# Kernel tuning notes

Measured on AMD Instinct MI355X. Metric: run time of the kernel, lower is better.

The kernel has to match this reference:

```python
import jax, jax.numpy as jnp
import numpy as np

UNITS = 50257
CUTOFF = [2000, 10000, UNITS]  # _cutoff = cutoff + [units]
C = 1024                        # channels (d_model)
N = 4096                        # flattened tokens (batch*seq)
N_TAILS = len(CUTOFF) - 1       # 2
ROOT_OUT = CUTOFF[0] + N_TAILS  # 2002
TAIL_DIMS = [256, 64]           # round(C/4**(i+1)/8)*8


def setup_inputs() -> dict:
    key = jax.random.key(0)
    ks = jax.random.split(key, 7)
    logits = jax.random.normal(ks[0], (N, C), jnp.float32)
    targets = jax.random.randint(ks[1], (N,), 0, UNITS, jnp.int32)
    s = 0.02
    head_kernel = jax.random.normal(ks[2], (C, ROOT_OUT), jnp.float32) * s
    proj0 = jax.random.normal(ks[3], (C, TAIL_DIMS[0]), jnp.float32) * s
    scale0 = jax.random.normal(ks[4], (TAIL_DIMS[0], CUTOFF[1] - CUTOFF[0]), jnp.float32) * s
    proj1 = jax.random.normal(ks[5], (C, TAIL_DIMS[1]), jnp.float32) * s
    scale1 = jax.random.normal(ks[6], (TAIL_DIMS[1], CUTOFF[2] - CUTOFF[1]), jnp.float32) * s
    return {"logits": logits, "targets": targets, "head_kernel": head_kernel,
            "proj0": proj0, "scale0": scale0, "proj1": proj1, "scale1": scale1}


def _sparse_ce(lg, labels):
    # sparse softmax cross entropy, numerically stable (single logsumexp)
    lse = jax.nn.logsumexp(lg, axis=-1)
    picked = jnp.take_along_axis(lg, labels[:, None].astype(jnp.int32), axis=1)[:, 0]
    return lse - picked


def reference(logits, targets, head_kernel, proj0, scale0, proj1, scale1):
    # Faithful jax version of AdaptiveSoftmax._train_loss (return_probs=False,
    # dropout=0, no bias on Denses, loss_reduction=SUM_OVER_BATCH_SIZE i.e. mean).
    # Dynamic boolean gather is replaced by dense compute + masked mean, which
    # yields identical math under jit (mean over the routed subset).
    root_logits = (logits @ head_kernel).astype(jnp.float32)  # [N, ROOT_OUT]
    root_targets = targets
    tails = [(proj0, scale0), (proj1, scale1)]
    losses = []
    for i, (p, s) in enumerate(tails):
        lo, hi = CUTOFF[i], CUTOFF[i + 1]
        m = (targets >= lo) & (targets < hi)
        root_targets = jnp.where(m, CUTOFF[0] + i, root_targets)
        tail_logits = ((logits @ p) @ s).astype(jnp.float32)  # [N, hi-lo]
        tail_tgt = jnp.clip(targets - lo, 0, hi - lo - 1)
        ce = _sparse_ce(tail_logits, tail_tgt)
        mf = m.astype(jnp.float32)
        losses.append(jnp.sum(ce * mf) / jnp.maximum(jnp.sum(mf), 1.0))
    root_loss = jnp.mean(_sparse_ce(root_logits, root_targets))
    all_losses = jnp.stack([root_loss] + losses)
    return jnp.mean(all_losses)
```

## Files before the change

kernel.cpp:

```cpp
#include <hip/hip_runtime.h>
#include <math.h>
#include <stdint.h>

#define NROWS 4096
#define CDIM 1024
#define T0_LO 2000
#define T0_HI 10000
#define T1_LO 10000
#define ROOT_COLS 2002
#define ROOT_PAD 2048
#define T0_COLS 8000
#define T0_PAD 8064
#define T1_COLS 40257
#define T1_PAD 40320
#define HB_STRIDE 320
#define LOG2E 1.44269504088896340736f
#define LN2 0.69314718055994530942f

using short8  = __attribute__((ext_vector_type(8))) short;
using ushort8 = __attribute__((ext_vector_type(8))) unsigned short;
using floatx4 = __attribute__((ext_vector_type(4))) float;

__device__ __forceinline__ unsigned short f2bf(float x) {
  union { float f; unsigned int u; } v; v.f = x;
  unsigned int r = v.u + 0x7fffu + ((v.u >> 16) & 1u);
  return (unsigned short)(r >> 16);
}
__device__ __forceinline__ float bf2f(unsigned short h) {
  union { unsigned int u; float f; } v; v.u = ((unsigned int)h) << 16;
  return v.f;
}
__device__ __forceinline__ floatx4 mfma16(short8 a, short8 b, floatx4 c) {
  return __builtin_amdgcn_mfma_f32_16x16x32_bf16(a, b, c, 0, 0, 0);
}
__device__ __forceinline__ void stage16(const unsigned short* g,
                                        unsigned short* lds_wave_base, int lane) {
#if __has_builtin(__builtin_amdgcn_global_load_lds)
  __builtin_amdgcn_global_load_lds(
      (const __attribute__((address_space(1))) void*)g,
      (__attribute__((address_space(3))) void*)lds_wave_base, 16, 0, 0);
#else
  ((ushort8*)lds_wave_base)[lane] = *(const ushort8*)g;
#endif
}

static constexpr size_t B_HB  = 0;
static constexpr size_t B_LB  = B_HB + 4096ull * 320 * 2;
static constexpr size_t B_WP  = B_LB + 4096ull * 1024 * 2;
static constexpr size_t B_WH  = B_WP + 384ull * 1024 * 2;
static constexpr size_t B_WS0 = B_WH + 2048ull * 1024 * 2;
static constexpr size_t B_WS1 = B_WS0 + 8064ull * 256 * 2;
static constexpr size_t B_S   = B_WS1 + 40320ull * 64 * 2;
static constexpr size_t B_P   = B_S + 3ull * 4096 * 4;
static constexpr size_t B_I0  = B_P + 3ull * 4096 * 4;
static constexpr size_t B_I1  = B_I0 + 4096ull * 4;
static constexpr size_t B_CNT = B_I1 + 4096ull * 4;

#define PR_WH_END   2048
#define PR_WP0_END  (PR_WH_END + 256)
#define PR_WP1_END  (PR_WP0_END + 64)
#define PR_WS0_END  (PR_WP1_END + 2016)
#define PR_WS1_END  (PR_WS0_END + 2520)
#define PR_ZERO_END (PR_WS1_END + 32)
#define PR_LB_END   (PR_ZERO_END + 2048)
#define PR_S_END    (PR_LB_END + 4)
#define PR_TOTAL    (PR_S_END + 1)

__global__ __launch_bounds__(256) void prep_kernel(
    const float* __restrict__ head, const float* __restrict__ proj0,
    const float* __restrict__ proj1, const float* __restrict__ scale0,
    const float* __restrict__ scale1, const float* __restrict__ logits,
    const int* __restrict__ targets,
    unsigned short* __restrict__ Wh, unsigned short* __restrict__ Wp,
    unsigned short* __restrict__ Ws0, unsigned short* __restrict__ Ws1,
    unsigned short* __restrict__ Lb, float* __restrict__ S,
    int* __restrict__ idx0, int* __restrict__ idx1, int* __restrict__ cnt) {
  const int id = blockIdx.x, tid = threadIdx.x;
  if (id >= PR_S_END) {
    __shared__ int base[2];
    if (tid < 2) base[tid] = 0;
    __syncthreads();
    for (int n = tid; n < NROWS; n += 256) {
      int t = targets[n];
      if (t >= T0_LO && t < T0_HI) idx0[atomicAdd(&base[0], 1)] = n;
      else if (t >= T1_LO)         idx1[atomicAdd(&base[1], 1)] = n;
    }
    __syncthreads();
    if (tid < 2) cnt[tid] = base[tid];
    return;
  }
  if (id >= PR_LB_END) {
    int rel = id - PR_LB_END;
    float4 z = make_float4(0.f, 0.f, 0.f, 0.f);
#pragma unroll
    for (int j = 0; j < 3; j++)
      ((float4*)S)[rel * 768 + j * 256 + tid] = z;
    return;
  }
  if (id >= PR_ZERO_END) {
    size_t base = (size_t)(id - PR_ZERO_END) * 2048 + tid * 8;
    float4 v0 = *(const float4*)(logits + base);
    float4 v1 = *(const float4*)(logits + base + 4);
    ushort8 h;
    h[0] = f2bf(v0.x); h[1] = f2bf(v0.y); h[2] = f2bf(v0.z); h[3] = f2bf(v0.w);
    h[4] = f2bf(v1.x); h[5] = f2bf(v1.y); h[6] = f2bf(v1.z); h[7] = f2bf(v1.w);
    *(ushort8*)(Lb + base) = h;
    return;
  }
  if (id >= PR_WS1_END) {
    size_t off = (size_t)(id - PR_WS1_END) * 2048 + tid * 8;
    ushort8 z = {0, 0, 0, 0, 0, 0, 0, 0};
    *(ushort8*)(Wp + 320ull * 1024 + off) = z;
    return;
  }
  const float* W; unsigned short* Wt; int K, N, Npad, nx, rel; float scale;
  if (id < PR_WH_END)       { W = head;   Wt = Wh;  K = 1024; N = ROOT_COLS; Npad = ROOT_PAD; scale = LOG2E; nx = 64;   rel = id; }
  else if (id < PR_WP0_END) { W = proj0;  Wt = Wp;  K = 1024; N = 256;  Npad = 256;  scale = 1.f;  nx = 8;    rel = id - PR_WH_END; }
  else if (id < PR_WP1_END) { W = proj1;  Wt = Wp + 256 * 1024; K = 1024; N = 64; Npad = 64; scale = 1.f; nx = 2; rel = id - PR_WP0_END; }
  else if (id < PR_WS0_END) { W = scale0; Wt = Ws0; K = 256;  N = T0_COLS; Npad = T0_PAD; scale = LOG2E; nx = 252;  rel = id - PR_WP1_END; }
  else                      { W = scale1; Wt = Ws1; K = 64;   N = T1_COLS; Npad = T1_PAD; scale = LOG2E; nx = 1260; rel = id - PR_WS0_END; }
  __shared__ float tile[32][33];
  const int n0 = (rel % nx) * 32, k0 = (rel / nx) * 32;
  const int tx = tid & 31, ty = tid >> 5;
  for (int i = 0; i < 32; i += 8) {
    int k = k0 + ty + i, n = n0 + tx;
    tile[ty + i][tx] = (n < N) ? W[(size_t)k * N + n] * scale : 0.f;
  }
  __syncthreads();
  const int nloc = tid >> 3, kg = tid & 7;
  const int n = n0 + nloc;
  if (n < Npad) {
    union { unsigned short v[4]; uint2 u; } x;
#pragma unroll
    for (int j = 0; j < 4; j++) x.v[j] = f2bf(tile[kg * 4 + j][nloc]);
    *(uint2*)&Wt[(size_t)n * K + k0 + kg * 4] = x.u;
  }
}

template<int CI>
__device__ __forceinline__ void gemm64_kloop(
    unsigned short* A_lds,
    const unsigned short* Arow,
    const unsigned short* const (&Bbase)[CI],
    floatx4 (&acc)[CI][4], int tid) {
  const int lane = tid & 63, w = tid >> 6;
  const int m = lane & 15, quad = lane >> 4, keym = m & 7;
  int goff[4];
#pragma unroll
  for (int it = 0; it < 4; it++) {
    int s = w * 256 + it * 64 + lane;
    int r = s >> 4, p = s & 15;
    int cq = p ^ (r & 7);
    goff[it] = r * CDIM + cq * 8;
  }
#pragma unroll
  for (int it = 0; it < 4; it++)
    stage16(Arow + goff[it], &A_lds[(w * 256 + it * 64) * 8], lane);
  for (int h = 0; h < 8; h++) {
    unsigned short* cur = A_lds + (h & 1) * (64 * 128);
    unsigned short* nxt = A_lds + ((h + 1) & 1) * (64 * 128);
    __syncthreads();
    if (h + 1 < 8) {
#pragma unroll
      for (int it = 0; it < 4; it++)
        stage16(Arow + goff[it] + (h + 1) * 128,
                &nxt[(w * 256 + it * 64) * 8], lane);
    }
    short8 b[CI][4];
#pragma unroll
    for (int ci = 0; ci < CI; ci++)
#pragma unroll
      for (int ks = 0; ks < 4; ks++)
        b[ci][ks] = *(const short8*)(Bbase[ci] + h * 128 + ks * 32);
    short8 areg[4][4];
#pragma unroll
    for (int t = 0; t < 4; t++)
#pragma unroll
      for (int ks = 0; ks < 4; ks++) {
        int ch = ((ks << 2) + quad) ^ keym;
        areg[t][ks] = *(const short8*)&cur[(t * 16 + m) * 128 + (ch << 3)];
      }
#pragma unroll
    for (int ci = 0; ci < CI; ci++)
#pragma unroll
      for (int ks = 0; ks < 4; ks++)
#pragma unroll
        for (int t = 0; t < 4; t++)
          acc[ci][t] = mfma16(areg[t][ks], b[ci][ks], acc[ci][t]);
  }
}

__global__ __launch_bounds__(256) void gemm_hidden(
    const unsigned short* __restrict__ Lb,
    const unsigned short* __restrict__ Wp,
    unsigned short* __restrict__ Hb) {
  __shared__ unsigned short A_lds[64 * 256];
  const int tid = threadIdx.x;
  const int row0 = blockIdx.x * 64;
  const int cg0 = blockIdx.y;
  const int lane = tid & 63, w = tid >> 6;
  const int m = lane & 15, quad = lane >> 4;
  const floatx4 zf = {0.f, 0.f, 0.f, 0.f};
  floatx4 acc[1][4];
#pragma unroll
  for (int t = 0; t < 4; t++) acc[0][t] = zf;
  const unsigned short* Bb[1] = {
      Wp + (size_t)(cg0 * 64 + w * 16 + m) * CDIM + quad * 8};
  gemm64_kloop<1>(A_lds, Lb + (size_t)row0 * CDIM, Bb, acc, tid);
  int n = cg0 * 64 + w * 16 + m;
  if (n < HB_STRIDE) {
#pragma unroll
    for (int t = 0; t < 4; t++)
#pragma unroll
      for (int r = 0; r < 4; r++)
        Hb[(size_t)(row0 + t * 16 + quad * 4 + r) * HB_STRIDE + n] =
            f2bf(acc[0][t][r]);
  }
}

#define MG_ROOT 512
#define MG_T1   480
#define MG_T0   2688
#define MG_PICK 1024
#define MG_TOTAL (MG_ROOT + MG_T1 + MG_T0 + MG_PICK)

__device__ __forceinline__ void root_path(
    unsigned char* smem, int bx, int by,
    const unsigned short* __restrict__ Lb,
    const unsigned short* __restrict__ Wh, float* __restrict__ S) {
  unsigned short* A_lds = (unsigned short*)smem;
  const int tid = threadIdx.x;
  const int row0 = bx * 128;
  const int cg0 = by * 2;
  const int lane = tid & 63, w = tid >> 6;
  const int m = lane & 15, quad = lane >> 4, keym = m & 7;
  const floatx4 zf = {0.f, 0.f, 0.f, 0.f};
  floatx4 acc[2][8];
#pragma unroll
  for (int ci = 0; ci < 2; ci++)
#pragma unroll
    for (int t = 0; t < 8; t++) acc[ci][t] = zf;
  const unsigned short* Bb[2] = {
      Wh + (size_t)((cg0 + 0) * 64 + w * 16 + m) * CDIM + quad * 8,
      Wh + (size_t)((cg0 + 1) * 64 + w * 16 + m) * CDIM + quad * 8};
  const unsigned short* Arow = Lb + (size_t)row0 * CDIM;
  int goff[8];
#pragma unroll
  for (int it = 0; it < 8; it++) {
    int s = w * 512 + it * 64 + lane;
    int r = s >> 4, p = s & 15;
    int cq = p ^ (r & 7);
    goff[it] = r * CDIM + cq * 8;
  }
  for (int h = 0; h < 8; h++) {
    short8 b[2][4];
#pragma unroll
    for (int ci = 0; ci < 2; ci++)
#pragma unroll
      for (int ks = 0; ks < 4; ks++)
        b[ci][ks] = *(const short8*)(Bb[ci] + h * 128 + ks * 32);
    __syncthreads();
#pragma unroll
    for (int it = 0; it < 8; it++)
      stage16(Arow + goff[it] + h * 128, &A_lds[(w * 512 + it * 64) * 8], lane);
    __syncthreads();
    short8 areg[4][4];
#pragma unroll
    for (int t = 0; t < 4; t++)
#pragma unroll
      for (int ks = 0; ks < 4; ks++) {
        int ch = ((ks << 2) + quad) ^ keym;
        areg[t][ks] = *(const short8*)&A_lds[(t * 16 + m) * 128 + (ch << 3)];
      }
#pragma unroll
    for (int ci = 0; ci < 2; ci++)
#pragma unroll
      for (int ks = 0; ks < 4; ks++)
#pragma unroll
        for (int t = 0; t < 4; t++)
          acc[ci][t] = mfma16(areg[t][ks], b[ci][ks], acc[ci][t]);
#pragma unroll
    for (int t = 0; t < 4; t++)
#pragma unroll
      for (int ks = 0; ks < 4; ks++) {
        int ch = ((ks << 2) + quad) ^ keym;
        areg[t][ks] = *(const short8*)&A_lds[(64 + t * 16 + m) * 128 + (ch << 3)];
      }
#pragma unroll
    for (int ci = 0; ci < 2; ci++)
#pragma unroll
      for (int ks = 0; ks < 4; ks++)
#pragma unroll
        for (int t = 0; t < 4; t++)
          acc[ci][4 + t] = mfma16(areg[t][ks], b[ci][ks], acc[ci][4 + t]);
  }
  __syncthreads();
  float* sums = (float*)smem;
  if (tid < 128) sums[tid] = 0.f;
  __syncthreads();
#pragma unroll
  for (int t = 0; t < 8; t++)
#pragma unroll
    for (int r = 0; r < 4; r++) {
      float e = __builtin_amdgcn_exp2f(acc[0][t][r]) +
                __builtin_amdgcn_exp2f(acc[1][t][r]);
      e += __shfl_xor(e, 1); e += __shfl_xor(e, 2);
      e += __shfl_xor(e, 4); e += __shfl_xor(e, 8);
      if (m == 0)
        atomicAdd(&sums[(t >> 2) * 64 + (t & 3) * 16 + quad * 4 + r], e);
    }
  __syncthreads();
  if (tid < 128) atomicAdd(&S[row0 + tid], sums[tid]);
}

template<int K, int TILES, int MODE>
__device__ __forceinline__ void tail_path(
    unsigned char* smem, int bx, int by,
    const unsigned short* __restrict__ Hb, int acol0,
    const unsigned short* __restrict__ Wt, int ncgpb,
    const int* __restrict__ idx, const int* __restrict__ cnt,
    float* __restrict__ S) {
  constexpr int BM = TILES * 16;
  constexpr int CpR = K / 8;
  constexpr int KS = K / 32;
  unsigned short* A_lds = (unsigned short*)smem;
  int* row_lds = (int*)(smem + (size_t)BM * K * 2);
  float* sum_lds = (float*)(smem + (size_t)BM * K * 2 + BM * 4);
  const int tid = threadIdx.x;
  const int count = cnt[MODE - 1];
  const int row0 = bx * BM;
  if (row0 >= count) return;
  if (tid < BM) {
    int r = row0 + tid;
    row_lds[tid] = (r < count) ? idx[r] : -1;
    sum_lds[tid] = 0.f;
  }
  __syncthreads();
#pragma unroll
  for (int i = 0; i < BM * CpR / 256; i++) {
    int c = tid + 256 * i;
    int rl = c / CpR, cq = c % CpR;
    int row = row_lds[rl];
    ushort8 v = {0, 0, 0, 0, 0, 0, 0, 0};
    if (row >= 0) v = *(const ushort8*)(Hb + (size_t)row * HB_STRIDE + acol0 + cq * 8);
    *(ushort8*)&A_lds[rl * K + ((cq ^ (rl & 7)) << 3)] = v;
  }
  __syncthreads();
  const int lane = tid & 63, w = tid >> 6;
  const int m = lane & 15, quad = lane >> 4, keym = m & 7;
  const floatx4 zf = {0.f, 0.f, 0.f, 0.f};
  short8 areg[TILES][KS];
#pragma unroll
  for (int t = 0; t < TILES; t++)
#pragma unroll
    for (int ks = 0; ks < KS; ks++) {
      int ch = ((ks << 2) + quad) ^ keym;
      areg[t][ks] = *(const short8*)&A_lds[(t * 16 + m) * K + (ch << 3)];
    }
  float runsum[TILES][4];
#pragma unroll
  for (int t = 0; t < TILES; t++)
#pragma unroll
    for (int r = 0; r < 4; r++) runsum[t][r] = 0.f;

  const int cg0 = by * ncgpb;
  const unsigned short* Bp = Wt + (size_t)(cg0 * 64 + w * 16 + m) * K + quad * 8;
  short8 b0[KS], b1[KS];
#pragma unroll
  for (int ks = 0; ks < KS; ks++) b0[ks] = *(const short8*)(Bp + ks * 32);
#pragma unroll
  for (int ks = 0; ks < KS; ks++)
    b1[ks] = *(const short8*)(Bp + (size_t)64 * K + ks * 32);

  for (int cc = 0; cc < ncgpb; cc += 2) {
    floatx4 acc[TILES];
#pragma unroll
    for (int t = 0; t < TILES; t++) acc[t] = zf;
#pragma unroll
    for (int ks = 0; ks < KS; ks++)
#pragma unroll
      for (int t = 0; t < TILES; t++) acc[t] = mfma16(areg[t][ks], b0[ks], acc[t]);
    if (cc + 2 < ncgpb) {
      const unsigned short* p = Bp + (size_t)(cc + 2) * 64 * K;
#pragma unroll
      for (int ks = 0; ks < KS; ks++) b0[ks] = *(const short8*)(p + ks * 32);
    }
#pragma unroll
    for (int t = 0; t < TILES; t++)
#pragma unroll
      for (int r = 0; r < 4; r++)
        runsum[t][r] += __builtin_amdgcn_exp2f(acc[t][r]);

#pragma unroll
    for (int t = 0; t < TILES; t++) acc[t] = zf;
#pragma unroll
    for (int ks = 0; ks < KS; ks++)
#pragma unroll
      for (int t = 0; t < TILES; t++) acc[t] = mfma16(areg[t][ks], b1[ks], acc[t]);
    if (cc + 3 < ncgpb) {
      const unsigned short* p = Bp + (size_t)(cc + 3) * 64 * K;
#pragma unroll
      for (int ks = 0; ks < KS; ks++) b1[ks] = *(const short8*)(p + ks * 32);
    }
#pragma unroll
    for (int t = 0; t < TILES; t++)
#pragma unroll
      for (int r = 0; r < 4; r++)
        runsum[t][r] += __builtin_amdgcn_exp2f(acc[t][r]);
  }

#pragma unroll
  for (int t = 0; t < TILES; t++)
#pragma unroll
    for (int r = 0; r < 4; r++) {
      float e = runsum[t][r];
      e += __shfl_xor(e, 1); e += __shfl_xor(e, 2);
      e += __shfl_xor(e, 4); e += __shfl_xor(e, 8);
      if (m == 0) atomicAdd(&sum_lds[t * 16 + quad * 4 + r], e);
    }
  __syncthreads();
  if (tid < BM) {
    int row = row_lds[tid];
    if (row >= 0) atomicAdd(&S[row], sum_lds[tid]);
  }
}

__device__ __forceinline__ void picked_path(
    int rel, const float* __restrict__ logits, const int* __restrict__ targets,
    const unsigned short* __restrict__ Wh,
    const unsigned short* __restrict__ Ws0,
    const unsigned short* __restrict__ Ws1,
    const unsigned short* __restrict__ Hb, float* __restrict__ P) {
  const int tid = threadIdx.x, lane = tid & 63;
  const int row = rel * 4 + (tid >> 6);
  const int t = targets[row];
  const int tr = (t >= T0_LO && t < T0_HI) ? T0_LO : ((t >= T1_LO) ? T0_LO + 1 : t);
  const float* a = logits + (size_t)row * CDIM + lane * 16;
  const unsigned short* wr = Wh + (size_t)tr * CDIM + lane * 16;
  float acc = 0.f;
#pragma unroll
  for (int q = 0; q < 2; q++) {
    ushort8 wv = *(const ushort8*)(wr + q * 8);
    float4 a0 = ((const float4*)a)[q * 2];
    float4 a1 = ((const float4*)a)[q * 2 + 1];
    acc += a0.x * bf2f(wv[0]) + a0.y * bf2f(wv[1]) + a0.z * bf2f(wv[2]) + a0.w * bf2f(wv[3]);
    acc += a1.x * bf2f(wv[4]) + a1.y * bf2f(wv[5]) + a1.z * bf2f(wv[6]) + a1.w * bf2f(wv[7]);
  }
#pragma unroll
  for (int off = 1; off < 64; off <<= 1) acc += __shfl_xor(acc, off);
  if (lane == 0) P[row] = acc * LN2;
  if (t >= T0_LO) {
    float acc2 = 0.f;
    if (t < T0_HI) {
      const unsigned short* h = Hb + (size_t)row * HB_STRIDE + lane * 4;
      const unsigned short* w2 = Ws0 + (size_t)(t - T0_LO) * 256 + lane * 4;
#pragma unroll
      for (int j = 0; j < 4; j++) acc2 += bf2f(h[j]) * bf2f(w2[j]);
    } else {
      acc2 = bf2f(Hb[(size_t)row * HB_STRIDE + 256 + lane]) *
             bf2f(Ws1[(size_t)(t - T1_LO) * 64 + lane]);
    }
#pragma unroll
    for (int off = 1; off < 64; off <<= 1) acc2 += __shfl_xor(acc2, off);
    if (lane == 0) P[(t < T0_HI ? NROWS : 2 * NROWS) + row] = acc2 * LN2;
  }
}

__global__ __launch_bounds__(256, 2) void mega_kernel(
    const unsigned short* __restrict__ Lb,
    const unsigned short* __restrict__ Wh,
    const unsigned short* __restrict__ Ws0,
    const unsigned short* __restrict__ Ws1,
    const unsigned short* __restrict__ Hb,
    const float* __restrict__ logits, const int* __restrict__ targets,
    const int* __restrict__ idx0, const int* __restrict__ idx1,
    const int* __restrict__ cnt, float* __restrict__ S, float* __restrict__ P) {
  __shared__ __align__(16) unsigned char smem[32768];
  int bid = blockIdx.x;
  if (bid < MG_ROOT) {
    root_path(smem, bid & 31, bid >> 5, Lb, Wh, S);
    return;
  }
  bid -= MG_ROOT;
  if (bid < MG_T1) {
    tail_path<64, 8, 2>(smem, bid & 31, bid >> 5, Hb, 256, Ws1, 42, idx1, cnt,
                        S + 2 * NROWS);
    return;
  }
  bid -= MG_T1;
  if (bid < MG_T0) {
    tail_path<256, 2, 1>(smem, bid & 127, bid >> 7, Hb, 0, Ws0, 6, idx0, cnt,
                         S + NROWS);
    return;
  }
  bid -= MG_T0;
  picked_path(bid, logits, targets, Wh, Ws0, Ws1, Hb, P);
}

__global__ void loss_kernel(const int* __restrict__ targets,
                            const float* __restrict__ S,
                            const float* __restrict__ P,
                            float* __restrict__ out) {
  const int tid = threadIdx.x;
  float sr = 0.f, s0 = 0.f, s1 = 0.f, c0 = 0.f, c1 = 0.f;
  for (int n = tid; n < NROWS; n += 256) {
    int t = targets[n];
    sr += logf(S[n] - 46.f) - P[n];
    if (t >= T0_LO && t < T0_HI) { s0 += logf(S[NROWS + n] - 64.f) - P[NROWS + n]; c0 += 1.f; }
    else if (t >= T1_LO)         { s1 += logf(S[2 * NROWS + n] - 63.f) - P[2 * NROWS + n]; c1 += 1.f; }
  }
  for (int off = 32; off > 0; off >>= 1) {
    sr += __shfl_down(sr, off);
    s0 += __shfl_down(s0, off);
    s1 += __shfl_down(s1, off);
    c0 += __shfl_down(c0, off);
    c1 += __shfl_down(c1, off);
  }
  __shared__ float red[4][5];
  int wv = tid >> 6;
  if ((tid & 63) == 0) { red[wv][0] = sr; red[wv][1] = s0; red[wv][2] = s1; red[wv][3] = c0; red[wv][4] = c1; }
  __syncthreads();
  if (tid == 0) {
    sr = red[0][0] + red[1][0] + red[2][0] + red[3][0];
    s0 = red[0][1] + red[1][1] + red[2][1] + red[3][1];
    s1 = red[0][2] + red[1][2] + red[2][2] + red[3][2];
    c0 = red[0][3] + red[1][3] + red[2][3] + red[3][3];
    c1 = red[0][4] + red[1][4] + red[2][4] + red[3][4];
    float root_loss = sr / (float)NROWS;
    float l0 = s0 / fmaxf(c0, 1.f);
    float l1 = s1 / fmaxf(c1, 1.f);
    out[0] = (root_loss + l0 + l1) / 3.f;
  }
}

extern "C" void kernel_launch(void* const* d_in, const int* in_sizes, int n_in,
                              void* d_out, int out_size, void* d_ws, size_t ws_size,
                              hipStream_t stream) {
  const float* logits  = (const float*)d_in[0];
  const int*   targets = (const int*)d_in[1];
  const float* head    = (const float*)d_in[2];
  const float* proj0   = (const float*)d_in[3];
  const float* scale0  = (const float*)d_in[4];
  const float* proj1   = (const float*)d_in[5];
  const float* scale1  = (const float*)d_in[6];
  float* out = (float*)d_out;
  char* ws = (char*)d_ws;

  unsigned short* Hb  = (unsigned short*)(ws + B_HB);
  unsigned short* Lb  = (unsigned short*)(ws + B_LB);
  unsigned short* Wp  = (unsigned short*)(ws + B_WP);
  unsigned short* Wh  = (unsigned short*)(ws + B_WH);
  unsigned short* Ws0 = (unsigned short*)(ws + B_WS0);
  unsigned short* Ws1 = (unsigned short*)(ws + B_WS1);
  float* S = (float*)(ws + B_S);
  float* P = (float*)(ws + B_P);
  int* idx0 = (int*)(ws + B_I0);
  int* idx1 = (int*)(ws + B_I1);
  int* cnt  = (int*)(ws + B_CNT);

  prep_kernel<<<PR_TOTAL, 256, 0, stream>>>(head, proj0, proj1, scale0, scale1,
                                            logits, targets, Wh, Wp, Ws0, Ws1,
                                            Lb, S, idx0, idx1, cnt);
  gemm_hidden<<<dim3(64, 5), 256, 0, stream>>>(Lb, Wp, Hb);
  mega_kernel<<<MG_TOTAL, 256, 0, stream>>>(Lb, Wh, Ws0, Ws1, Hb, logits,
                                            targets, idx0, idx1, cnt, S, P);
  loss_kernel<<<1, 256, 0, stream>>>(targets, S, P, out);
}
```

Baseline: 209.5 us.

## Double-buffer root GEMM LDS, remap block IDs across XCDs, widen loss kernel

The root-path GEMM now uses two 64-wide K slices in LDS, loading the next A tile and B fragments while computing on the current one. This replaces the single-buffer stage-sync-compute loop and is meant to hide global-load latency. Block indices for the root and tail paths are permuted so that consecutive hardware block IDs, which round-robin across XCDs, map to neighbouring work tiles, aiming for better L2 reuse. The final loss reduction kernel runs with 1024 threads instead of 256.

```diff
diff --git a/kernel.cpp b/kernel.cpp
--- a/kernel.cpp
+++ b/kernel.cpp
@@ -224,11 +224,52 @@
 #define MG_PICK 1024
 #define MG_TOTAL (MG_ROOT + MG_T1 + MG_T0 + MG_PICK)
 
+__device__ __forceinline__ void root_compute(
+    const unsigned short* cur, const short8 (&b)[2][2], floatx4 (&acc)[2][8],
+    int m, int quad, int keym) {
+#pragma unroll
+  for (int hf = 0; hf < 2; hf++) {
+    short8 areg[4][2];
+#pragma unroll
+    for (int t = 0; t < 4; t++)
+#pragma unroll
+      for (int ks = 0; ks < 2; ks++) {
+        int ch = ((ks << 2) + quad) ^ keym;
+        areg[t][ks] = *(const short8*)&cur[(hf * 64 + t * 16 + m) * 64 + (ch << 3)];
+      }
+#pragma unroll
+    for (int ci = 0; ci < 2; ci++)
+#pragma unroll
+      for (int ks = 0; ks < 2; ks++)
+#pragma unroll
+        for (int t = 0; t < 4; t++)
+          acc[ci][hf * 4 + t] = mfma16(areg[t][ks], b[ci][ks], acc[ci][hf * 4 + t]);
+  }
+}
+
+__device__ __forceinline__ void root_stage(
+    const unsigned short* Arow, const int (&goff)[4], int koff,
+    unsigned short* buf, int w, int lane) {
+#pragma unroll
+  for (int it = 0; it < 4; it++)
+    stage16(Arow + goff[it] + koff, &buf[(it * 256 + w * 64) * 8], lane);
+}
+
+__device__ __forceinline__ void root_loadB(
+    const unsigned short* const (&Bb)[2], int koff, short8 (&b)[2][2]) {
+#pragma unroll
+  for (int ci = 0; ci < 2; ci++)
+#pragma unroll
+    for (int ks = 0; ks < 2; ks++)
+      b[ci][ks] = *(const short8*)(Bb[ci] + koff + ks * 32);
+}
+
 __device__ __forceinline__ void root_path(
     unsigned char* smem, int bx, int by,
     const unsigned short* __restrict__ Lb,
     const unsigned short* __restrict__ Wh, float* __restrict__ S) {
-  unsigned short* A_lds = (unsigned short*)smem;
+  unsigned short* bufA = (unsigned short*)smem;
+  unsigned short* bufB = bufA + 128 * 64;
   const int tid = threadIdx.x;
   const int row0 = bx * 128;
   const int cg0 = by * 2;
@@ -244,55 +285,28 @@
       Wh + (size_t)((cg0 + 0) * 64 + w * 16 + m) * CDIM + quad * 8,
       Wh + (size_t)((cg0 + 1) * 64 + w * 16 + m) * CDIM + quad * 8};
   const unsigned short* Arow = Lb + (size_t)row0 * CDIM;
-  int goff[8];
-#pragma unroll
-  for (int it = 0; it < 8; it++) {
-    int s = w * 512 + it * 64 + lane;
-    int r = s >> 4, p = s & 15;
+  int goff[4];
+#pragma unroll
+  for (int it = 0; it < 4; it++) {
+    int s = it * 256 + w * 64 + lane;
+    int r = s >> 3, p = s & 7;
     int cq = p ^ (r & 7);
     goff[it] = r * CDIM + cq * 8;
   }
-  for (int h = 0; h < 8; h++) {
-    short8 b[2][4];
-#pragma unroll
-    for (int ci = 0; ci < 2; ci++)
-#pragma unroll
-      for (int ks = 0; ks < 4; ks++)
-        b[ci][ks] = *(const short8*)(Bb[ci] + h * 128 + ks * 32);
+  short8 b0[2][2], b1[2][2];
+  root_stage(Arow, goff, 0, bufA, w, lane);
+  root_loadB(Bb, 0, b0);
+  for (int hh = 0; hh < 8; hh++) {
     __syncthreads();
-#pragma unroll
-    for (int it = 0; it < 8; it++)
-      stage16(Arow + goff[it] + h * 128, &A_lds[(w * 512 + it * 64) * 8], lane);
+    root_stage(Arow, goff, (hh * 2 + 1) * 64, bufB, w, lane);
+    root_loadB(Bb, (hh * 2 + 1) * 64, b1);
+    root_compute(bufA, b0, acc, m, quad, keym);
     __syncthreads();
-    short8 areg[4][4];
-#pragma unroll
-    for (int t = 0; t < 4; t++)
-#pragma unroll
-      for (int ks = 0; ks < 4; ks++) {
-        int ch = ((ks << 2) + quad) ^ keym;
-        areg[t][ks] = *(const short8*)&A_lds[(t * 16 + m) * 128 + (ch << 3)];
-      }
-#pragma unroll
-    for (int ci = 0; ci < 2; ci++)
-#pragma unroll
-      for (int ks = 0; ks < 4; ks++)
-#pragma unroll
-        for (int t = 0; t < 4; t++)
-          acc[ci][t] = mfma16(areg[t][ks], b[ci][ks], acc[ci][t]);
-#pragma unroll
-    for (int t = 0; t < 4; t++)
-#pragma unroll
-      for (int ks = 0; ks < 4; ks++) {
-        int ch = ((ks << 2) + quad) ^ keym;
-        areg[t][ks] = *(const short8*)&A_lds[(64 + t * 16 + m) * 128 + (ch << 3)];
-      }
-#pragma unroll
-    for (int ci = 0; ci < 2; ci++)
-#pragma unroll
-      for (int ks = 0; ks < 4; ks++)
-#pragma unroll
-        for (int t = 0; t < 4; t++)
-          acc[ci][4 + t] = mfma16(areg[t][ks], b[ci][ks], acc[ci][4 + t]);
+    if (hh < 7) {
+      root_stage(Arow, goff, (hh * 2 + 2) * 64, bufA, w, lane);
+      root_loadB(Bb, (hh * 2 + 2) * 64, b0);
+    }
+    root_compute(bufB, b1, acc, m, quad, keym);
   }
   __syncthreads();
   float* sums = (float*)smem;
@@ -478,18 +492,21 @@
   __shared__ __align__(16) unsigned char smem[32768];
   int bid = blockIdx.x;
   if (bid < MG_ROOT) {
-    root_path(smem, bid & 31, bid >> 5, Lb, Wh, S);
+    int wk = ((bid & 7) << 6) + (bid >> 3);
+    root_path(smem, wk >> 4, wk & 15, Lb, Wh, S);
     return;
   }
   bid -= MG_ROOT;
   if (bid < MG_T1) {
-    tail_path<64, 8, 2>(smem, bid & 31, bid >> 5, Hb, 256, Ws1, 42, idx1, cnt,
+    int wk = (bid & 7) * 60 + (bid >> 3);
+    tail_path<64, 8, 2>(smem, wk & 31, wk >> 5, Hb, 256, Ws1, 42, idx1, cnt,
                         S + 2 * NROWS);
     return;
   }
   bid -= MG_T1;
   if (bid < MG_T0) {
-    tail_path<256, 2, 1>(smem, bid & 127, bid >> 7, Hb, 0, Ws0, 6, idx0, cnt,
+    int wk = (bid & 7) * 336 + (bid >> 3);
+    tail_path<256, 2, 1>(smem, wk & 127, wk >> 7, Hb, 0, Ws0, 6, idx0, cnt,
                          S + NROWS);
     return;
   }
@@ -497,13 +514,14 @@
   picked_path(bid, logits, targets, Wh, Ws0, Ws1, Hb, P);
 }
 
-__global__ void loss_kernel(const int* __restrict__ targets,
-                            const float* __restrict__ S,
-                            const float* __restrict__ P,
-                            float* __restrict__ out) {
+__global__ __launch_bounds__(1024) void loss_kernel(
+    const int* __restrict__ targets,
+    const float* __restrict__ S,
+    const float* __restrict__ P,
+    float* __restrict__ out) {
   const int tid = threadIdx.x;
   float sr = 0.f, s0 = 0.f, s1 = 0.f, c0 = 0.f, c1 = 0.f;
-  for (int n = tid; n < NROWS; n += 256) {
+  for (int n = tid; n < NROWS; n += 1024) {
     int t = targets[n];
     sr += logf(S[n] - 46.f) - P[n];
     if (t >= T0_LO && t < T0_HI) { s0 += logf(S[NROWS + n] - 64.f) - P[NROWS + n]; c0 += 1.f; }
@@ -516,16 +534,17 @@
     c0 += __shfl_down(c0, off);
     c1 += __shfl_down(c1, off);
   }
-  __shared__ float red[4][5];
+  __shared__ float red[16][5];
   int wv = tid >> 6;
   if ((tid & 63) == 0) { red[wv][0] = sr; red[wv][1] = s0; red[wv][2] = s1; red[wv][3] = c0; red[wv][4] = c1; }
   __syncthreads();
   if (tid == 0) {
-    sr = red[0][0] + red[1][0] + red[2][0] + red[3][0];
-    s0 = red[0][1] + red[1][1] + red[2][1] + red[3][1];
-    s1 = red[0][2] + red[1][2] + red[2][2] + red[3][2];
-    c0 = red[0][3] + red[1][3] + red[2][3] + red[3][3];
-    c1 = red[0][4] + red[1][4] + red[2][4] + red[3][4];
+    sr = 0.f; s0 = 0.f; s1 = 0.f; c0 = 0.f; c1 = 0.f;
+#pragma unroll
+    for (int i = 0; i < 16; i++) {
+      sr += red[i][0]; s0 += red[i][1]; s1 += red[i][2];
+      c0 += red[i][3]; c1 += red[i][4];
+    }
     float root_loss = sr / (float)NROWS;
     float l0 = s0 / fmaxf(c0, 1.f);
     float l1 = s1 / fmaxf(c1, 1.f);
@@ -564,5 +583,5 @@
   gemm_hidden<<<dim3(64, 5), 256, 0, stream>>>(Lb, Wp, Hb);
   mega_kernel<<<MG_TOTAL, 256, 0, stream>>>(Lb, Wh, Ws0, Ws1, Hb, logits,
                                             targets, idx0, idx1, cnt, S, P);
-  loss_kernel<<<1, 256, 0, stream>>>(targets, S, P, out);
-}
+  loss_kernel<<<1, 1024, 0, stream>>>(targets, S, P, out);
+}
```

Measured after the change: 191.4 us. 8.6% less time.
